# Optimization experiments

Hardware: AMD Instinct MI355X
Metric: run time of the kernel (lower is better)

## Reference

```python
import jax, jax.numpy as jnp
import numpy as np

N, K, C, OUT = 50000, 16, 128, 128
PAD_FRAC = 0.1  # fraction of neighbor slots masked with -1


def setup_inputs() -> dict:
    key = jax.random.key(0)
    k1, k2, k3, k4, k5 = jax.random.split(key, 5)
    x = jax.random.normal(k1, (N, C), dtype=jnp.float32)
    edge_index = jax.random.randint(k2, (N, K), 0, N)
    drop = jax.random.uniform(k3, (N, K)) < PAD_FRAC
    drop = drop.at[:, 0].set(False)  # keep >=1 valid neighbor per node
    edge_index = jnp.where(drop, -1, edge_index)
    W = jax.random.normal(k4, (2 * C, OUT), dtype=jnp.float32) / np.sqrt(2.0 * C)
    b = jax.random.normal(k5, (OUT,), dtype=jnp.float32) * 0.01
    return {"x": x, "edge_index": edge_index, "W": W, "b": b}


def reference(x, edge_index, W, b):
    # Pad node table with a zero row; index -1 wraps to it (matches torch's
    # node_feature_padded[edge_index] with explicit -1 -> zeros semantics).
    padded = jnp.concatenate([x, jnp.zeros((1, x.shape[1]), x.dtype)], axis=0)
    neigh = padded[edge_index]                      # [N, K, C]
    xr = x[:, None, :]                              # [N, 1, C]
    h = jnp.concatenate(
        [jnp.broadcast_to(xr, neigh.shape), neigh - xr], axis=-1
    )                                               # [N, K, 2C]
    out = jax.nn.elu(jnp.einsum('nkc,co->nko', h, W) + b)  # [N, K, OUT]
    out = jnp.where(edge_index[..., None] != -1, out, -jnp.inf)
    return jnp.max(out, axis=1)                     # [N, OUT]
```

## Files before the change

### kernel.cpp

```cpp
#include <hip/hip_runtime.h>
#include <hip/hip_bf16.h>
#include <hip/hip_fp16.h>
#include <math.h>

#define NNODES 50000
#define KNEI 16

typedef __attribute__((ext_vector_type(8))) short bf8;
typedef __attribute__((ext_vector_type(4))) float f32x4;

static __device__ __forceinline__ unsigned short f2bf(float f) {
    __hip_bfloat16 h = __float2bfloat16(f);
    return *reinterpret_cast<unsigned short*>(&h);
}
static __device__ __forceinline__ unsigned short f2h(float f) {
    __half h = __float2half(f);
    return *reinterpret_cast<unsigned short*>(&h);
}
static __device__ __forceinline__ float2 h2f2(unsigned int u) {
    __half2 h = *reinterpret_cast<__half2*>(&u);
    return __half22float2(h);
}

__global__ __launch_bounds__(128) void prep_bt(const float* __restrict__ W,
                                               unsigned short* __restrict__ BT) {
    int c = blockIdx.x;
    int k = threadIdx.x;
    float v;
    if (c < 128) v = W[k * 128 + c] - W[(k + 128) * 128 + c];
    else         v = W[(k + 128) * 128 + (c - 128)];
    BT[c * 128 + k] = f2bf(v);
}

__global__ __launch_bounds__(256) void gemm_bf16(const float* __restrict__ x,
                                                 const unsigned short* __restrict__ BT,
                                                 const float* __restrict__ bias,
                                                 unsigned short* __restrict__ Ph,
                                                 unsigned short* __restrict__ Qh) {
    __shared__ unsigned short Ls[64 * 264];
    const int t = threadIdx.x;
    const int row0 = blockIdx.x * 64;

    #pragma unroll
    for (int i = 0; i < 8; ++i) {
        int f  = t + i * 256;
        int r  = f >> 5;
        int c4 = f & 31;
        int gr = row0 + r;
        float4 v = make_float4(0.f, 0.f, 0.f, 0.f);
        if (gr < NNODES) v = ((const float4*)x)[gr * 32 + c4];
        unsigned int u0 = (unsigned int)f2bf(v.x) | ((unsigned int)f2bf(v.y) << 16);
        unsigned int u1 = (unsigned int)f2bf(v.z) | ((unsigned int)f2bf(v.w) << 16);
        *(uint2*)&Ls[r * 136 + c4 * 4] = make_uint2(u0, u1);
    }
    __syncthreads();

    const int w  = t >> 6;
    const int l  = t & 63;
    const int lr = l & 15;
    const int lk = (l >> 4) * 8;

    f32x4 acc[4][4];
    #pragma unroll
    for (int m = 0; m < 4; ++m)
        #pragma unroll
        for (int n = 0; n < 4; ++n) acc[m][n] = (f32x4){0.f, 0.f, 0.f, 0.f};

    const int colG0 = w * 64 + lr;
    const unsigned short* bt0 = BT + colG0 * 128 + lk;

    #pragma unroll
    for (int s = 0; s < 4; ++s) {
        const int kp = s * 32;
        bf8 a[4], b[4];
        #pragma unroll
        for (int m = 0; m < 4; ++m)
            a[m] = *(const bf8*)&Ls[(m * 16 + lr) * 136 + kp + lk];
        #pragma unroll
        for (int n = 0; n < 4; ++n)
            b[n] = *(const bf8*)(bt0 + n * 16 * 128 + kp);
        #pragma unroll
        for (int m = 0; m < 4; ++m)
            #pragma unroll
            for (int n = 0; n < 4; ++n)
                acc[m][n] = __builtin_amdgcn_mfma_f32_16x16x32_bf16(a[m], b[n], acc[m][n], 0, 0, 0);
    }

    float bb[4];
    #pragma unroll
    for (int n = 0; n < 4; ++n) {
        int col = colG0 + n * 16;
        bb[n] = (col < 128) ? bias[col] : 0.f;
    }

    __syncthreads();
    #pragma unroll
    for (int m = 0; m < 4; ++m) {
        #pragma unroll
        for (int n = 0; n < 4; ++n) {
            int cg = colG0 + n * 16;
            #pragma unroll
            for (int i = 0; i < 4; ++i) {
                int rl = m * 16 + (l >> 4) * 4 + i;
                Ls[rl * 264 + cg] = f2h(acc[m][n][i] + bb[n]);
            }
        }
    }
    __syncthreads();

    #pragma unroll
    for (int it = 0; it < 8; ++it) {
        int cidx = t + it * 256;
        int row  = cidx >> 5;
        int seg  = cidx & 31;
        uint4 v = *(const uint4*)&Ls[row * 264 + seg * 8];
        int gr = row0 + row;
        if (gr < NNODES) {
            int col = seg * 8;
            if (col < 128)
                *(uint4*)(Ph + (size_t)gr * 128 + col) = v;
            else
                *(uint4*)(Qh + (size_t)gr * 128 + (col - 128)) = v;
        }
    }
}

__global__ __launch_bounds__(256) void gather_max(const unsigned short* __restrict__ Ph,
                                                  const unsigned short* __restrict__ Qh,
                                                  const int* __restrict__ edge,
                                                  float* __restrict__ out) {
    const int t  = threadIdx.x;
    const int n  = blockIdx.x * 16 + (t >> 4);
    const int o8 = (t & 15) * 8;

    const int4* er = (const int4*)(edge + n * KNEI);
    int4 e0 = er[0], e1 = er[1], e2 = er[2], e3 = er[3];
    int ia[16] = {e0.x, e0.y, e0.z, e0.w, e1.x, e1.y, e1.z, e1.w,
                  e2.x, e2.y, e2.z, e2.w, e3.x, e3.y, e3.z, e3.w};
    const int s0 = ia[0];
    const unsigned short* qb = Qh + o8;

    uint4 q[16];
    #pragma unroll
    for (int k = 0; k < 16; ++k) {
        int ix = ia[k] < 0 ? s0 : ia[k];
        q[k] = *(const uint4*)(qb + (size_t)ix * 128);
    }
    uint4 pv = *(const uint4*)(Ph + (size_t)n * 128 + o8);

    float2 m0 = h2f2(q[0].x), m1 = h2f2(q[0].y), m2 = h2f2(q[0].z), m3 = h2f2(q[0].w);
    #pragma unroll
    for (int k = 1; k < 16; ++k) {
        float2 a0 = h2f2(q[k].x), a1 = h2f2(q[k].y), a2 = h2f2(q[k].z), a3 = h2f2(q[k].w);
        m0.x = fmaxf(m0.x, a0.x); m0.y = fmaxf(m0.y, a0.y);
        m1.x = fmaxf(m1.x, a1.x); m1.y = fmaxf(m1.y, a1.y);
        m2.x = fmaxf(m2.x, a2.x); m2.y = fmaxf(m2.y, a2.y);
        m3.x = fmaxf(m3.x, a3.x); m3.y = fmaxf(m3.y, a3.y);
    }
    float2 p0 = h2f2(pv.x), p1 = h2f2(pv.y), p2 = h2f2(pv.z), p3 = h2f2(pv.w);

    float z[8] = {p0.x + m0.x, p0.y + m0.y, p1.x + m1.x, p1.y + m1.y,
                  p2.x + m2.x, p2.y + m2.y, p3.x + m3.x, p3.y + m3.y};
    float r[8];
    #pragma unroll
    for (int i = 0; i < 8; ++i) r[i] = z[i] > 0.f ? z[i] : expm1f(z[i]);

    float* ob = out + (size_t)n * 128 + o8;
    *(float4*)ob       = make_float4(r[0], r[1], r[2], r[3]);
    *(float4*)(ob + 4) = make_float4(r[4], r[5], r[6], r[7]);
}

extern "C" void kernel_launch(void* const* d_in, const int* in_sizes, int n_in,
                              void* d_out, int out_size, void* d_ws, size_t ws_size,
                              hipStream_t stream) {
    const float* x    = (const float*)d_in[0];
    const int*   edge = (const int*)d_in[1];
    const float* W    = (const float*)d_in[2];
    const float* bias = (const float*)d_in[3];
    float* out = (float*)d_out;

    unsigned short* Qh = (unsigned short*)d_ws;
    unsigned short* Ph = Qh + 6400000;
    unsigned short* BT = Qh + 12800000;

    prep_bt<<<256, 128, 0, stream>>>(W, BT);
    gemm_bf16<<<(NNODES + 63) / 64, 256, 0, stream>>>(x, BT, bias, Ph, Qh);
    gather_max<<<NNODES / 16, 256, 0, stream>>>(Ph, Qh, edge, out);
}
```

Before: 122.7 us.

## Process two tiles per GEMM block with register prefetch and direct global stores

```diff
diff --git a/kernel.cpp b/kernel.cpp
--- a/kernel.cpp
+++ b/kernel.cpp
@@ -5,6 +5,7 @@
 
 #define NNODES 50000
 #define KNEI 16
+#define GBLK 391
 
 typedef __attribute__((ext_vector_type(8))) short bf8;
 typedef __attribute__((ext_vector_type(4))) float f32x4;
@@ -37,54 +38,14 @@
                                                  const float* __restrict__ bias,
                                                  unsigned short* __restrict__ Ph,
                                                  unsigned short* __restrict__ Qh) {
-    __shared__ unsigned short Ls[64 * 264];
-    const int t = threadIdx.x;
-    const int row0 = blockIdx.x * 64;
-
-    #pragma unroll
-    for (int i = 0; i < 8; ++i) {
-        int f  = t + i * 256;
-        int r  = f >> 5;
-        int c4 = f & 31;
-        int gr = row0 + r;
-        float4 v = make_float4(0.f, 0.f, 0.f, 0.f);
-        if (gr < NNODES) v = ((const float4*)x)[gr * 32 + c4];
-        unsigned int u0 = (unsigned int)f2bf(v.x) | ((unsigned int)f2bf(v.y) << 16);
-        unsigned int u1 = (unsigned int)f2bf(v.z) | ((unsigned int)f2bf(v.w) << 16);
-        *(uint2*)&Ls[r * 136 + c4 * 4] = make_uint2(u0, u1);
-    }
-    __syncthreads();
-
+    __shared__ unsigned short S[64 * 136];
+    const int t  = threadIdx.x;
     const int w  = t >> 6;
     const int l  = t & 63;
     const int lr = l & 15;
     const int lk = (l >> 4) * 8;
-
-    f32x4 acc[4][4];
-    #pragma unroll
-    for (int m = 0; m < 4; ++m)
-        #pragma unroll
-        for (int n = 0; n < 4; ++n) acc[m][n] = (f32x4){0.f, 0.f, 0.f, 0.f};
-
     const int colG0 = w * 64 + lr;
     const unsigned short* bt0 = BT + colG0 * 128 + lk;
-
-    #pragma unroll
-    for (int s = 0; s < 4; ++s) {
-        const int kp = s * 32;
-        bf8 a[4], b[4];
-        #pragma unroll
-        for (int m = 0; m < 4; ++m)
-            a[m] = *(const bf8*)&Ls[(m * 16 + lr) * 136 + kp + lk];
-        #pragma unroll
-        for (int n = 0; n < 4; ++n)
-            b[n] = *(const bf8*)(bt0 + n * 16 * 128 + kp);
-        #pragma unroll
-        for (int m = 0; m < 4; ++m)
-            #pragma unroll
-            for (int n = 0; n < 4; ++n)
-                acc[m][n] = __builtin_amdgcn_mfma_f32_16x16x32_bf16(a[m], b[n], acc[m][n], 0, 0, 0);
-    }
 
     float bb[4];
     #pragma unroll
@@ -93,35 +54,88 @@
         bb[n] = (col < 128) ? bias[col] : 0.f;
     }
 
-    __syncthreads();
-    #pragma unroll
-    for (int m = 0; m < 4; ++m) {
-        #pragma unroll
-        for (int n = 0; n < 4; ++n) {
-            int cg = colG0 + n * 16;
-            #pragma unroll
-            for (int i = 0; i < 4; ++i) {
-                int rl = m * 16 + (l >> 4) * 4 + i;
-                Ls[rl * 264 + cg] = f2h(acc[m][n][i] + bb[n]);
+    int tile = blockIdx.x;
+
+    float4 R[8];
+    {
+        const int row0 = tile * 64;
+        #pragma unroll
+        for (int i = 0; i < 8; ++i) {
+            int f  = t + i * 256;
+            int r  = f >> 5;
+            int c4 = f & 31;
+            int gr = row0 + r;
+            R[i] = (gr < NNODES) ? ((const float4*)x)[gr * 32 + c4]
+                                 : make_float4(0.f, 0.f, 0.f, 0.f);
+        }
+    }
+
+    #pragma unroll
+    for (int it = 0; it < 2; ++it) {
+        const int row0 = tile * 64;
+
+        __syncthreads();
+        #pragma unroll
+        for (int i = 0; i < 8; ++i) {
+            int f  = t + i * 256;
+            int r  = f >> 5;
+            int c4 = f & 31;
+            unsigned int u0 = (unsigned int)f2bf(R[i].x) | ((unsigned int)f2bf(R[i].y) << 16);
+            unsigned int u1 = (unsigned int)f2bf(R[i].z) | ((unsigned int)f2bf(R[i].w) << 16);
+            *(uint2*)&S[r * 136 + c4 * 4] = make_uint2(u0, u1);
+        }
+        if (it == 0) {
+            const int prow0 = (tile + GBLK) * 64;
+            #pragma unroll
+            for (int i = 0; i < 8; ++i) {
+                int f  = t + i * 256;
+                int r  = f >> 5;
+                int c4 = f & 31;
+                int gr = prow0 + r;
+                R[i] = (gr < NNODES) ? ((const float4*)x)[gr * 32 + c4]
+                                     : make_float4(0.f, 0.f, 0.f, 0.f);
             }
         }
-    }
-    __syncthreads();
-
-    #pragma unroll
-    for (int it = 0; it < 8; ++it) {
-        int cidx = t + it * 256;
-        int row  = cidx >> 5;
-        int seg  = cidx & 31;
-        uint4 v = *(const uint4*)&Ls[row * 264 + seg * 8];
-        int gr = row0 + row;
-        if (gr < NNODES) {
-            int col = seg * 8;
-            if (col < 128)
-                *(uint4*)(Ph + (size_t)gr * 128 + col) = v;
-            else
-                *(uint4*)(Qh + (size_t)gr * 128 + (col - 128)) = v;
-        }
+        __syncthreads();
+
+        f32x4 acc[4][4];
+        #pragma unroll
+        for (int m = 0; m < 4; ++m)
+            #pragma unroll
+            for (int n = 0; n < 4; ++n) acc[m][n] = (f32x4){0.f, 0.f, 0.f, 0.f};
+
+        #pragma unroll
+        for (int s = 0; s < 4; ++s) {
+            const int kp = s * 32;
+            bf8 a[4], b[4];
+            #pragma unroll
+            for (int m = 0; m < 4; ++m)
+                a[m] = *(const bf8*)&S[(m * 16 + lr) * 136 + kp + lk];
+            #pragma unroll
+            for (int n = 0; n < 4; ++n)
+                b[n] = *(const bf8*)(bt0 + n * 16 * 128 + kp);
+            #pragma unroll
+            for (int m = 0; m < 4; ++m)
+                #pragma unroll
+                for (int n = 0; n < 4; ++n)
+                    acc[m][n] = __builtin_amdgcn_mfma_f32_16x16x32_bf16(a[m], b[n], acc[m][n], 0, 0, 0);
+        }
+
+        #pragma unroll
+        for (int m = 0; m < 4; ++m) {
+            #pragma unroll
+            for (int n = 0; n < 4; ++n) {
+                const int col = colG0 + n * 16;
+                unsigned short* base = (col < 128) ? (Ph + col) : (Qh + (col - 128));
+                #pragma unroll
+                for (int i = 0; i < 4; ++i) {
+                    int row = row0 + m * 16 + (l >> 4) * 4 + i;
+                    if (row < NNODES)
+                        base[(size_t)row * 128] = f2h(acc[m][n][i] + bb[n]);
+                }
+            }
+        }
+        tile += GBLK;
     }
 }
 
@@ -184,6 +198,6 @@
     unsigned short* BT = Qh + 12800000;
 
     prep_bt<<<256, 128, 0, stream>>>(W, BT);
-    gemm_bf16<<<(NNODES + 63) / 64, 256, 0, stream>>>(x, BT, bias, Ph, Qh);
+    gemm_bf16<<<GBLK, 256, 0, stream>>>(x, BT, bias, Ph, Qh);
     gather_max<<<NNODES / 16, 256, 0, stream>>>(Ph, Qh, edge, out);
 }
```

After: 119.5 us. -2.6%, faster.

## Precompute bf16 copy of x and drop LDS staging in GEMM epilogue

Applied to the files above, without the earlier changes.

```diff
diff --git a/kernel.cpp b/kernel.cpp
--- a/kernel.cpp
+++ b/kernel.cpp
@@ -4,14 +4,15 @@
 #include <math.h>
 
 #define NNODES 50000
+#define NPAD   50048
 #define KNEI 16
 
 typedef __attribute__((ext_vector_type(8))) short bf8;
 typedef __attribute__((ext_vector_type(4))) float f32x4;
 
-static __device__ __forceinline__ unsigned short f2bf(float f) {
+static __device__ __forceinline__ unsigned int f2bf(float f) {
     __hip_bfloat16 h = __float2bfloat16(f);
-    return *reinterpret_cast<unsigned short*>(&h);
+    return (unsigned int)*reinterpret_cast<unsigned short*>(&h);
 }
 static __device__ __forceinline__ unsigned short f2h(float f) {
     __half h = __float2half(f);
@@ -29,36 +30,47 @@
     float v;
     if (c < 128) v = W[k * 128 + c] - W[(k + 128) * 128 + c];
     else         v = W[(k + 128) * 128 + (c - 128)];
-    BT[c * 128 + k] = f2bf(v);
+    BT[c * 128 + k] = (unsigned short)f2bf(v);
 }
 
-__global__ __launch_bounds__(256) void gemm_bf16(const float* __restrict__ x,
+__global__ __launch_bounds__(256) void prep_xb(const float* __restrict__ x,
+                                               unsigned short* __restrict__ xb) {
+    size_t e = ((size_t)blockIdx.x * 256 + threadIdx.x) * 8;
+    int row = (int)(e >> 7);
+    uint4 o = make_uint4(0, 0, 0, 0);
+    if (row < NNODES) {
+        float4 v0 = *(const float4*)&x[e];
+        float4 v1 = *(const float4*)&x[e + 4];
+        o.x = f2bf(v0.x) | (f2bf(v0.y) << 16);
+        o.y = f2bf(v0.z) | (f2bf(v0.w) << 16);
+        o.z = f2bf(v1.x) | (f2bf(v1.y) << 16);
+        o.w = f2bf(v1.z) | (f2bf(v1.w) << 16);
+    }
+    *(uint4*)&xb[e] = o;
+}
+
+__global__ __launch_bounds__(256) void gemm_bf16(const unsigned short* __restrict__ xb,
                                                  const unsigned short* __restrict__ BT,
                                                  const float* __restrict__ bias,
                                                  unsigned short* __restrict__ Ph,
                                                  unsigned short* __restrict__ Qh) {
-    __shared__ unsigned short Ls[64 * 264];
-    const int t = threadIdx.x;
-    const int row0 = blockIdx.x * 64;
-
-    #pragma unroll
-    for (int i = 0; i < 8; ++i) {
-        int f  = t + i * 256;
-        int r  = f >> 5;
-        int c4 = f & 31;
-        int gr = row0 + r;
-        float4 v = make_float4(0.f, 0.f, 0.f, 0.f);
-        if (gr < NNODES) v = ((const float4*)x)[gr * 32 + c4];
-        unsigned int u0 = (unsigned int)f2bf(v.x) | ((unsigned int)f2bf(v.y) << 16);
-        unsigned int u1 = (unsigned int)f2bf(v.z) | ((unsigned int)f2bf(v.w) << 16);
-        *(uint2*)&Ls[r * 136 + c4 * 4] = make_uint2(u0, u1);
-    }
-    __syncthreads();
-
+    const int t  = threadIdx.x;
     const int w  = t >> 6;
     const int l  = t & 63;
     const int lr = l & 15;
     const int lk = (l >> 4) * 8;
+    const int row0 = blockIdx.x * 64;
+    const int colG0 = w * 64 + lr;
+
+    const unsigned short* bt0 = BT + colG0 * 128 + lk;
+    const unsigned short* a0  = xb + (size_t)(row0 + lr) * 128 + lk;
+
+    float bb[4];
+    #pragma unroll
+    for (int n = 0; n < 4; ++n) {
+        int col = colG0 + n * 16;
+        bb[n] = (col < 128) ? bias[col] : 0.f;
+    }
 
     f32x4 acc[4][4];
     #pragma unroll
@@ -66,16 +78,13 @@
         #pragma unroll
         for (int n = 0; n < 4; ++n) acc[m][n] = (f32x4){0.f, 0.f, 0.f, 0.f};
 
-    const int colG0 = w * 64 + lr;
-    const unsigned short* bt0 = BT + colG0 * 128 + lk;
-
     #pragma unroll
     for (int s = 0; s < 4; ++s) {
         const int kp = s * 32;
         bf8 a[4], b[4];
         #pragma unroll
         for (int m = 0; m < 4; ++m)
-            a[m] = *(const bf8*)&Ls[(m * 16 + lr) * 136 + kp + lk];
+            a[m] = *(const bf8*)(a0 + (size_t)m * 16 * 128 + kp);
         #pragma unroll
         for (int n = 0; n < 4; ++n)
             b[n] = *(const bf8*)(bt0 + n * 16 * 128 + kp);
@@ -86,41 +95,18 @@
                 acc[m][n] = __builtin_amdgcn_mfma_f32_16x16x32_bf16(a[m], b[n], acc[m][n], 0, 0, 0);
     }
 
-    float bb[4];
-    #pragma unroll
-    for (int n = 0; n < 4; ++n) {
-        int col = colG0 + n * 16;
-        bb[n] = (col < 128) ? bias[col] : 0.f;
-    }
-
-    __syncthreads();
     #pragma unroll
     for (int m = 0; m < 4; ++m) {
         #pragma unroll
         for (int n = 0; n < 4; ++n) {
-            int cg = colG0 + n * 16;
+            const int col = colG0 + n * 16;
+            unsigned short* base = (col < 128) ? (Ph + col) : (Qh + (col - 128));
             #pragma unroll
             for (int i = 0; i < 4; ++i) {
-                int rl = m * 16 + (l >> 4) * 4 + i;
-                Ls[rl * 264 + cg] = f2h(acc[m][n][i] + bb[n]);
+                int row = row0 + m * 16 + (l >> 4) * 4 + i;
+                if (row < NNODES)
+                    base[(size_t)row * 128] = f2h(acc[m][n][i] + bb[n]);
             }
-        }
-    }
-    __syncthreads();
-
-    #pragma unroll
-    for (int it = 0; it < 8; ++it) {
-        int cidx = t + it * 256;
-        int row  = cidx >> 5;
-        int seg  = cidx & 31;
-        uint4 v = *(const uint4*)&Ls[row * 264 + seg * 8];
-        int gr = row0 + row;
-        if (gr < NNODES) {
-            int col = seg * 8;
-            if (col < 128)
-                *(uint4*)(Ph + (size_t)gr * 128 + col) = v;
-            else
-                *(uint4*)(Qh + (size_t)gr * 128 + (col - 128)) = v;
         }
     }
 }
@@ -182,8 +168,10 @@
     unsigned short* Qh = (unsigned short*)d_ws;
     unsigned short* Ph = Qh + 6400000;
     unsigned short* BT = Qh + 12800000;
+    unsigned short* xb = Qh + 12832768;
 
     prep_bt<<<256, 128, 0, stream>>>(W, BT);
-    gemm_bf16<<<(NNODES + 63) / 64, 256, 0, stream>>>(x, BT, bias, Ph, Qh);
+    prep_xb<<<(NPAD * 128) / (8 * 256), 256, 0, stream>>>(x, xb);
+    gemm_bf16<<<NPAD / 64, 256, 0, stream>>>(xb, BT, bias, Ph, Qh);
     gather_max<<<NNODES / 16, 256, 0, stream>>>(Ph, Qh, edge, out);
 }
```

Result: slower. 131.5 us (+7.2%).
